# Optimization experiments

Hardware: AMD Instinct MI355X
Metric: run time of the kernel (lower is better)

Reference implementation:

```python
import jax, jax.numpy as jnp
import numpy as np

NU = 100_000   # users
NI = 100_000   # items
D  = 64        # embedding_size
NR = 1_000_000 # rate edges (user->item)
NL = 500_000   # link edges (user->user)
NEG_SLOPE = 0.2


def setup_inputs() -> dict:
    key = jax.random.key(0)
    ks = iter(jax.random.split(key, 40))
    s1 = 1.0 / np.sqrt(D)      # fan-in D
    s2 = 1.0 / np.sqrt(2 * D)  # fan-in 2D
    def nrm(shape, scale):
        return (jax.random.normal(next(ks), shape, jnp.float32) * scale).astype(jnp.float32)
    def idx(n, hi):
        return jax.random.randint(next(ks), (n,), 0, hi, jnp.int32)
    inp = {
        "user_emb": nrm((NU, D), 0.1),
        "item_emb": nrm((NI, D), 0.1),
        "rate_src": idx(NR, NU), "rate_dst": idx(NR, NI),
        "link_src": idx(NL, NU), "link_dst": idx(NL, NU),
        "neg_rate_src": idx(NR, NU), "neg_rate_dst": idx(NR, NI),
        "neg_link_src": idx(NL, NU), "neg_link_dst": idx(NL, NU),
        "lambda_max": jnp.full((), 2.0, jnp.float32),
        "gat_Wsrc": nrm((5, D, D), s1), "gat_bsrc": nrm((5, D), s1),
        "gat_Wdst": nrm((5, D, D), s1), "gat_bdst": nrm((5, D), s1),
        "gat_attn": nrm((5, D), s1),
        "W_out": nrm((2 * D, D), s2), "b_out": nrm((D,), s2),
        "cheb_W": nrm((3, D, D), s1), "cheb_b": nrm((D,), s1),
        "Wc": nrm((2 * D, D), s2), "bc": nrm((D,), s2),
        "Ws": nrm((2 * D, D), s2), "bs": nrm((D,), s2),
        "WpP": nrm((2 * D, D), s2), "bpP": nrm((D,), s2),
        "WpS": nrm((2 * D, D), s2), "bpS": nrm((D,), s2),
    }
    return inp


def _gatv2(Wsrc, bsrc, Wdst, bdst, attn, h_src, h_dst, src, dst, n_dst):
    """DGL GATv2Conv, num_heads=1, head dim squeezed. Returns [n_dst, D]."""
    fs = h_src @ Wsrc + bsrc            # [Ns, D]
    fd = h_dst @ Wdst + bdst            # [Nd, D]
    e = jax.nn.leaky_relu(fs[src] + fd[dst], NEG_SLOPE)  # [E, D]
    s = e @ attn                        # [E]
    m = jax.ops.segment_max(s, dst, num_segments=n_dst)
    ex = jnp.exp(s - m[dst])
    den = jax.ops.segment_sum(ex, dst, num_segments=n_dst)
    alpha = ex / den[dst]               # edge softmax per dst node
    return jax.ops.segment_sum(alpha[:, None] * fs[src], dst, num_segments=n_dst)


def _forward(user_emb, item_emb, rate_src, rate_dst, link_src, link_dst,
             neg_rate_src, neg_rate_dst, neg_link_src, neg_link_dst,
             lambda_max, gat_Wsrc, gat_bsrc, gat_Wdst, gat_bdst, gat_attn,
             W_out, b_out, cheb_W, cheb_b, Wc, bc, Ws, bs, WpP, bpP, WpS, bpS):
    def gat(i, h_src, h_dst, src, dst, n_dst):
        return _gatv2(gat_Wsrc[i], gat_bsrc[i], gat_Wdst[i], gat_bdst[i],
                      gat_attn[i], h_src, h_dst, src, dst, n_dst)

    # ---- SpatialAttentionLayer_GAT ----
    h1_item = gat(0, user_emb, item_emb, rate_src, rate_dst, NI)      # layer1[rate]
    h2_user = gat(1, item_emb, user_emb, rate_dst, rate_src, NU)      # layer1[rated-by]
    item_infl = gat(2, h1_item, user_emb, rate_dst, rate_src, NU)     # layer2[rated-by]
    social_item = gat(3, h2_user, user_emb, link_src, link_dst, NU)   # layer2[link]
    user_pref = jnp.concatenate([item_infl, social_item], axis=1) @ W_out + b_out

    # ---- SpectralAttentionLayer: ChebConv(k=3) on social graph + GATv2 ----
    indeg = jax.ops.segment_sum(jnp.ones((NL,), jnp.float32), link_dst, num_segments=NU)
    dinv = jnp.maximum(indeg, 1.0) ** -0.5
    def ahat(x):  # D^{-1/2} A D^{-1/2} x over link edges
        msg = (x * dinv[:, None])[link_src]
        return dinv[:, None] * jax.ops.segment_sum(msg, link_dst, num_segments=NU)
    re = 2.0 / lambda_max
    T0 = user_emb
    rst = T0 @ cheb_W[0]
    h = ahat(T0)
    T1 = -re * h + T0 * (re - 1.0)
    rst = rst + T1 @ cheb_W[1]
    h = ahat(T1)
    T2 = -2.0 * re * h + 2.0 * (re - 1.0) * T1 - T0
    rst = rst + T2 @ cheb_W[2] + cheb_b
    user_social = gat(4, rst, rst, link_src, link_dst, NU)

    # ---- MutualisicLayer ----
    h_uP = jnp.concatenate([user_pref, user_emb], axis=1) @ Wc + bc
    h_uS = jnp.concatenate([user_social, user_emb], axis=1) @ Ws + bs
    h_m = h_uP * h_uS
    h_mP = h_m * jax.nn.softmax(h_uP, axis=1)
    h_mS = h_m * jax.nn.softmax(h_uS, axis=1)
    h_miu_mP = jnp.concatenate([h_mP, h_uP], axis=1)
    h_miu_mS = jnp.concatenate([h_mS, h_uS], axis=1)

    # ---- PredictionLayer ----
    h_new_P = h_miu_mP @ WpP + bpP
    h_new_S = h_miu_mS @ WpS + bpS

    # ---- HeteroDotProductPredictor (u_dot_v per edge) ----
    pos_rate = jnp.sum(h_new_P[rate_src] * item_emb[rate_dst], axis=-1)
    neg_rate = jnp.sum(h_new_P[neg_rate_src] * item_emb[neg_rate_dst], axis=-1)
    pos_link = jnp.sum(h_new_S[link_src] * user_emb[link_dst], axis=-1)
    neg_link = jnp.sum(h_new_S[neg_link_src] * user_emb[neg_link_dst], axis=-1)
    return pos_rate, neg_rate, pos_link, neg_link


def reference(user_emb, item_emb, rate_src, rate_dst, link_src, link_dst,
              neg_rate_src, neg_rate_dst, neg_link_src, neg_link_dst,
              lambda_max, gat_Wsrc, gat_bsrc, gat_Wdst, gat_bdst, gat_attn,
              W_out, b_out, cheb_W, cheb_b, Wc, bc, Ws, bs, WpP, bpP, WpS, bpS):
    return _forward(user_emb, item_emb, rate_src, rate_dst, link_src, link_dst,
                    neg_rate_src, neg_rate_dst, neg_link_src, neg_link_dst,
                    lambda_max, gat_Wsrc, gat_bsrc, gat_Wdst, gat_bdst, gat_attn,
                    W_out, b_out, cheb_W, cheb_b, Wc, bc, Ws, bs, WpP, bpP, WpS, bpS)
```

## Files before the change

kernel.cpp:

```cpp
#include <hip/hip_runtime.h>


#define LRELU_SLOPE 0.2f
#define MFMA_BLOCKS 1024
#define EDGE_BLOCKS 2048

typedef unsigned short u16;
typedef unsigned int uint32;
typedef __attribute__((ext_vector_type(8))) short short8;
typedef __attribute__((ext_vector_type(4))) float f32x4;

__device__ __forceinline__ float b2f(u16 u) {
  return __uint_as_float(((uint32)u) << 16);
}
__device__ __forceinline__ u16 f2b(float f) {
  uint32 u = __float_as_uint(f);
  uint32 r = (u + 0x7fffu + ((u >> 16) & 1u)) >> 16;
  return (u16)r;
}
__device__ __forceinline__ float blo(uint32 p) { return __uint_as_float(p << 16); }
__device__ __forceinline__ float bhi(uint32 p) { return __uint_as_float(p & 0xffff0000u); }
__device__ __forceinline__ uint32 packb(float lo, float hi) {
  return (uint32)f2b(lo) | ((uint32)f2b(hi) << 16);
}

__global__ void cvt_k(const float4* __restrict__ X, ushort4* __restrict__ Y, int n4) {
  const int stride = gridDim.x * blockDim.x;
  for (int i = blockIdx.x * blockDim.x + threadIdx.x; i < n4; i += stride) {
    const float4 v = X[i];
    ushort4 o;
    o.x = f2b(v.x); o.y = f2b(v.y); o.z = f2b(v.z); o.w = f2b(v.w);
    Y[i] = o;
  }
}

__global__ void wfrag_k(const float* __restrict__ W, u16* __restrict__ fb, int nmat) {
  const int total = nmat * 4096;
  const int stride = gridDim.x * blockDim.x;
  for (int i = blockIdx.x * blockDim.x + threadIdx.x; i < total; i += stride) {
    const int mat = i >> 12, rem = i & 4095;
    const int l = rem >> 6, r = rem & 63;
    const int kc = r >> 5, cb = (r >> 3) & 3, j = r & 7;
    const int k = kc * 32 + ((l >> 4) & 3) * 8 + j;
    const int col = cb * 16 + (l & 15);
    fb[i] = f2b(W[(size_t)mat * 4096 + k * 64 + col]);
  }
}

template <int NIN>
__global__ void mfma_g_k(const u16* __restrict__ X0, const u16* __restrict__ X1,
                         const u16* __restrict__ X2,
                         const u16* __restrict__ F0, const u16* __restrict__ F1,
                         const u16* __restrict__ F2,
                         const float* __restrict__ b, u16* __restrict__ Y, int N) {
  const int lane = threadIdx.x & 63;
  const int gw = (blockIdx.x * blockDim.x + threadIdx.x) >> 6;
  const int nw = (gridDim.x * blockDim.x) >> 6;
  const int lo = lane & 15, hi = lane >> 4;
  short8 bf[NIN][2][4];
#pragma unroll
  for (int i = 0; i < NIN; ++i) {
    const u16* Fi = (i == 0) ? F0 : ((i == 1) ? F1 : F2);
#pragma unroll
    for (int kc = 0; kc < 2; ++kc)
#pragma unroll
      for (int cb = 0; cb < 4; ++cb)
        bf[i][kc][cb] = *(const short8*)(Fi + (size_t)lane * 64 + kc * 32 + cb * 8);
  }
  float bcol[4];
#pragma unroll
  for (int cb = 0; cb < 4; ++cb) bcol[cb] = b[cb * 16 + lo];
  const int ntile = (N + 15) >> 4;
  for (int t = gw; t < ntile; t += nw) {
    int arow = t * 16 + lo;
    if (arow >= N) arow = N - 1;
    f32x4 acc[4];
#pragma unroll
    for (int cb = 0; cb < 4; ++cb) {
      acc[cb][0] = bcol[cb]; acc[cb][1] = bcol[cb];
      acc[cb][2] = bcol[cb]; acc[cb][3] = bcol[cb];
    }
#pragma unroll
    for (int i = 0; i < NIN; ++i) {
      const u16* Xi = (i == 0) ? X0 : ((i == 1) ? X1 : X2);
      const short8 a0 = *(const short8*)(Xi + (size_t)arow * 64 + hi * 8);
      const short8 a1 = *(const short8*)(Xi + (size_t)arow * 64 + 32 + hi * 8);
#pragma unroll
      for (int cb = 0; cb < 4; ++cb)
        acc[cb] = __builtin_amdgcn_mfma_f32_16x16x32_bf16(a0, bf[i][0][cb], acc[cb], 0, 0, 0);
#pragma unroll
      for (int cb = 0; cb < 4; ++cb)
        acc[cb] = __builtin_amdgcn_mfma_f32_16x16x32_bf16(a1, bf[i][1][cb], acc[cb], 0, 0, 0);
    }
#pragma unroll
    for (int cb = 0; cb < 4; ++cb) {
#pragma unroll
      for (int j = 0; j < 4; ++j) {
        const int row = t * 16 + hi * 4 + j;
        if (row < N) Y[(size_t)row * 64 + cb * 16 + lo] = f2b(acc[cb][j]);
      }
    }
  }
}

__global__ void hist_k(const int* __restrict__ key, int* __restrict__ cnt, int E) {
  const int e = blockIdx.x * blockDim.x + threadIdx.x;
  if (e < E) atomicAdd(cnt + key[e], 1);
}

__global__ void scan1_k(const int* __restrict__ in, int* __restrict__ out,
                        int* __restrict__ bsum, int n) {
  __shared__ int tmp[256];
  const int t = threadIdx.x;
  const int base = blockIdx.x * 1024 + t * 4;
  int v0 = (base + 0 < n) ? in[base + 0] : 0;
  int v1 = (base + 1 < n) ? in[base + 1] : 0;
  int v2 = (base + 2 < n) ? in[base + 2] : 0;
  int v3 = (base + 3 < n) ? in[base + 3] : 0;
  const int s = v0 + v1 + v2 + v3;
  tmp[t] = s;
  __syncthreads();
  for (int off = 1; off < 256; off <<= 1) {
    const int x = (t >= off) ? tmp[t - off] : 0;
    __syncthreads();
    tmp[t] += x;
    __syncthreads();
  }
  const int excl = tmp[t] - s;
  if (t == 255) bsum[blockIdx.x] = tmp[255];
  if (base + 0 < n) out[base + 0] = excl;
  if (base + 1 < n) out[base + 1] = excl + v0;
  if (base + 2 < n) out[base + 2] = excl + v0 + v1;
  if (base + 3 < n) out[base + 3] = excl + v0 + v1 + v2;
}
__global__ void scan2_k(int* __restrict__ bsum, int nb) {
  if (threadIdx.x == 0) {
    int acc = 0;
    for (int i = 0; i < nb; ++i) { const int v = bsum[i]; bsum[i] = acc; acc += v; }
  }
}
__global__ void scan3_k(int* __restrict__ out, const int* __restrict__ bsum, int n) {
  const int i = blockIdx.x * blockDim.x + threadIdx.x;
  if (i < n) out[i] += bsum[i >> 10];
}

__global__ void scatter_k(const int* __restrict__ key, const int* __restrict__ other,
                          int* __restrict__ cursor, int* __restrict__ srt, int E) {
  const int e = blockIdx.x * blockDim.x + threadIdx.x;
  if (e < E) {
    const int p = atomicAdd(cursor + key[e], 1);
    srt[p] = other[e];
  }
}

__global__ void gat32_k(const u16* __restrict__ fs, const u16* __restrict__ fd,
                        const float* __restrict__ attn,
                        const int* __restrict__ rowptr, const int* __restrict__ nbr,
                        u16* __restrict__ out, int N) {
  const int lane = threadIdx.x & 63;
  const int l = lane & 31, half = lane >> 5;
  const int wid = (blockIdx.x * blockDim.x + threadIdx.x) >> 6;
  const int nw = (gridDim.x * blockDim.x) >> 6;
  const float awlo = attn[2 * l], awhi = attn[2 * l + 1];
  const uint32* fs32 = (const uint32*)fs;
  const uint32* fd32 = (const uint32*)fd;
  uint32* out32 = (uint32*)out;
  for (int n0 = wid * 2; n0 < N; n0 += nw * 2) {
    const int n = n0 + half;
    const bool act = n < N;
    const int beg = act ? rowptr[n] : 0;
    const int end = act ? rowptr[n + 1] : 0;
    float fdlo = 0.0f, fdhi = 0.0f;
    if (act) {
      const uint32 fp = fd32[(size_t)n * 32 + l];
      fdlo = blo(fp); fdhi = bhi(fp);
    }
    float aclo = 0.0f, achi = 0.0f, den = 0.0f;
    int e = beg;
    for (; e + 1 < end; e += 2) {
      const int s0 = nbr[e], s1 = nbr[e + 1];
      const uint32 f0 = fs32[(size_t)s0 * 32 + l];
      const uint32 f1 = fs32[(size_t)s1 * 32 + l];
      const float f0l = blo(f0), f0h = bhi(f0);
      const float f1l = blo(f1), f1h = bhi(f1);
      float v0l = f0l + fdlo; v0l = v0l > 0.0f ? v0l : LRELU_SLOPE * v0l;
      float v0h = f0h + fdhi; v0h = v0h > 0.0f ? v0h : LRELU_SLOPE * v0h;
      float v1l = f1l + fdlo; v1l = v1l > 0.0f ? v1l : LRELU_SLOPE * v1l;
      float v1h = f1h + fdhi; v1h = v1h > 0.0f ? v1h : LRELU_SLOPE * v1h;
      float p0 = fmaf(v0l, awlo, v0h * awhi);
      float p1 = fmaf(v1l, awlo, v1h * awhi);
#pragma unroll
      for (int o = 16; o; o >>= 1) {
        p0 += __shfl_xor(p0, o, 64);
        p1 += __shfl_xor(p1, o, 64);
      }
      const float e0 = __expf(p0), e1 = __expf(p1);
      den += e0 + e1;
      aclo = fmaf(e0, f0l, aclo); achi = fmaf(e0, f0h, achi);
      aclo = fmaf(e1, f1l, aclo); achi = fmaf(e1, f1h, achi);
    }
    if (e < end) {
      const int s0 = nbr[e];
      const uint32 f0 = fs32[(size_t)s0 * 32 + l];
      const float f0l = blo(f0), f0h = bhi(f0);
      float v0l = f0l + fdlo; v0l = v0l > 0.0f ? v0l : LRELU_SLOPE * v0l;
      float v0h = f0h + fdhi; v0h = v0h > 0.0f ? v0h : LRELU_SLOPE * v0h;
      float p0 = fmaf(v0l, awlo, v0h * awhi);
#pragma unroll
      for (int o = 16; o; o >>= 1) p0 += __shfl_xor(p0, o, 64);
      const float e0 = __expf(p0);
      den += e0;
      aclo = fmaf(e0, f0l, aclo); achi = fmaf(e0, f0h, achi);
    }
    const float inv = den > 0.0f ? 1.0f / den : 0.0f;
    if (act) out32[(size_t)n * 32 + l] = packb(aclo * inv, achi * inv);
  }
}

template <int MODE>
__global__ void cheb32_k(const u16* __restrict__ x, const u16* __restrict__ T0,
                         const u16* __restrict__ Tp, const float* __restrict__ dinv,
                         const float* __restrict__ lam,
                         const int* __restrict__ rowptr, const int* __restrict__ nbr,
                         u16* __restrict__ outT, int N) {
  const float re = 2.0f / lam[0];
  const int lane = threadIdx.x & 63;
  const int l = lane & 31, half = lane >> 5;
  const int wid = (blockIdx.x * blockDim.x + threadIdx.x) >> 6;
  const int nw = (gridDim.x * blockDim.x) >> 6;
  const uint32* x32 = (const uint32*)x;
  const uint32* T032 = (const uint32*)T0;
  const uint32* Tp32 = (const uint32*)Tp;
  uint32* o32 = (uint32*)outT;
  for (int n0 = wid * 2; n0 < N; n0 += nw * 2) {
    const int n = n0 + half;
    const bool act = n < N;
    const int beg = act ? rowptr[n] : 0;
    const int end = act ? rowptr[n + 1] : 0;
    float aclo = 0.0f, achi = 0.0f;
    int e = beg;
    for (; e + 1 < end; e += 2) {
      const int s0 = nbr[e], s1 = nbr[e + 1];
      const uint32 f0 = x32[(size_t)s0 * 32 + l];
      const uint32 f1 = x32[(size_t)s1 * 32 + l];
      const float d0 = dinv[s0], d1 = dinv[s1];
      aclo = fmaf(blo(f0), d0, aclo); achi = fmaf(bhi(f0), d0, achi);
      aclo = fmaf(blo(f1), d1, aclo); achi = fmaf(bhi(f1), d1, achi);
    }
    if (e < end) {
      const int s0 = nbr[e];
      const uint32 f0 = x32[(size_t)s0 * 32 + l];
      const float d0 = dinv[s0];
      aclo = fmaf(blo(f0), d0, aclo); achi = fmaf(bhi(f0), d0, achi);
    }
    if (!act) continue;
    const float dn = dinv[n];
    const float hl = aclo * dn, hh = achi * dn;
    float rl, rh;
    if (MODE == 1) {
      const uint32 t0 = T032[(size_t)n * 32 + l];
      rl = -re * hl + (re - 1.0f) * blo(t0);
      rh = -re * hh + (re - 1.0f) * bhi(t0);
    } else {
      const uint32 t0 = T032[(size_t)n * 32 + l];
      const uint32 tp = Tp32[(size_t)n * 32 + l];
      rl = -2.0f * re * hl + 2.0f * (re - 1.0f) * blo(tp) - blo(t0);
      rh = -2.0f * re * hh + 2.0f * (re - 1.0f) * bhi(tp) - bhi(t0);
    }
    o32[(size_t)n * 32 + l] = packb(rl, rh);
  }
}

__global__ void dinv_k(const int* __restrict__ rowptr, float* __restrict__ dinv, int N) {
  const int i = blockIdx.x * blockDim.x + threadIdx.x;
  if (i < N) {
    const float deg = (float)(rowptr[i + 1] - rowptr[i]);
    dinv[i] = rsqrtf(fmaxf(deg, 1.0f));
  }
}

__global__ void mut_k(const u16* __restrict__ hP, const u16* __restrict__ hS,
                      u16* __restrict__ mP, u16* __restrict__ mS, int N) {
  const int lane = threadIdx.x & 63;
  const int u = (blockIdx.x * blockDim.x + threadIdx.x) >> 6;
  if (u >= N) return;
  const float p = b2f(hP[(size_t)u * 64 + lane]);
  const float s = b2f(hS[(size_t)u * 64 + lane]);
  const float m = p * s;
  float mxp = p, mxs = s;
#pragma unroll
  for (int o = 32; o; o >>= 1) {
    mxp = fmaxf(mxp, __shfl_xor(mxp, o, 64));
    mxs = fmaxf(mxs, __shfl_xor(mxs, o, 64));
  }
  const float ep = __expf(p - mxp);
  const float es = __expf(s - mxs);
  float sp = ep, ss = es;
#pragma unroll
  for (int o = 32; o; o >>= 1) {
    sp += __shfl_xor(sp, o, 64);
    ss += __shfl_xor(ss, o, 64);
  }
  mP[(size_t)u * 64 + lane] = f2b(m * (ep / sp));
  mS[(size_t)u * 64 + lane] = f2b(m * (es / ss));
}

__global__ void dot32_k(const u16* __restrict__ A, const u16* __restrict__ Bm,
                        const int* __restrict__ src, const int* __restrict__ dst,
                        float* __restrict__ out, int E) {
  const int lane = threadIdx.x & 63;
  const int l = lane & 31, half = lane >> 5;
  const int wid = (blockIdx.x * blockDim.x + threadIdx.x) >> 6;
  const int nw = (gridDim.x * blockDim.x) >> 6;
  const uint32* A32 = (const uint32*)A;
  const uint32* B32 = (const uint32*)Bm;
  for (int e0 = wid * 4; e0 < E; e0 += nw * 4) {
    const int eA = e0 + half;
    const int eB = e0 + 2 + half;
    const int eAc = eA < E ? eA : E - 1;
    const int eBc = eB < E ? eB : E - 1;
    const int sA = src[eAc], dA = dst[eAc];
    const int sB = src[eBc], dB = dst[eBc];
    const uint32 a0 = A32[(size_t)sA * 32 + l];
    const uint32 b0 = B32[(size_t)dA * 32 + l];
    const uint32 a1 = A32[(size_t)sB * 32 + l];
    const uint32 b1 = B32[(size_t)dB * 32 + l];
    float p0 = fmaf(blo(a0), blo(b0), bhi(a0) * bhi(b0));
    float p1 = fmaf(blo(a1), blo(b1), bhi(a1) * bhi(b1));
#pragma unroll
    for (int o = 16; o; o >>= 1) {
      p0 += __shfl_xor(p0, o, 64);
      p1 += __shfl_xor(p1, o, 64);
    }
    if (l == 0) {
      if (eA < E) out[eA] = p0;
      if (eB < E) out[eB] = p1;
    }
  }
}


static void build_csr(const int* key, const int* other, int E, int N,
                      int* rowptr, int* srt, int* cursor, int* bsum,
                      hipStream_t stream) {
  const int n1 = N + 1;
  hipMemsetAsync(cursor, 0, (size_t)n1 * 4, stream);
  hist_k<<<(E + 255) / 256, 256, 0, stream>>>(key, cursor, E);
  const int nb = (n1 + 1023) / 1024;
  scan1_k<<<nb, 256, 0, stream>>>(cursor, rowptr, bsum, n1);
  scan2_k<<<1, 64, 0, stream>>>(bsum, nb);
  scan3_k<<<(n1 + 255) / 256, 256, 0, stream>>>(rowptr, bsum, n1);
  hipMemcpyAsync(cursor, rowptr, (size_t)N * 4, hipMemcpyDeviceToDevice, stream);
  scatter_k<<<(E + 255) / 256, 256, 0, stream>>>(key, other, cursor, srt, E);
}

extern "C" void kernel_launch(void* const* d_in, const int* in_sizes, int n_in,
                              void* d_out, int out_size, void* d_ws, size_t ws_size,
                              hipStream_t stream) {
  const float* user_emb = (const float*)d_in[0];
  const float* item_emb = (const float*)d_in[1];
  const int* rate_src = (const int*)d_in[2];
  const int* rate_dst = (const int*)d_in[3];
  const int* link_src = (const int*)d_in[4];
  const int* link_dst = (const int*)d_in[5];
  const int* neg_rate_src = (const int*)d_in[6];
  const int* neg_rate_dst = (const int*)d_in[7];
  const int* neg_link_src = (const int*)d_in[8];
  const int* neg_link_dst = (const int*)d_in[9];
  const float* lam = (const float*)d_in[10];
  const float* gat_Wsrc = (const float*)d_in[11];
  const float* gat_bsrc = (const float*)d_in[12];
  const float* gat_Wdst = (const float*)d_in[13];
  const float* gat_bdst = (const float*)d_in[14];
  const float* gat_attn = (const float*)d_in[15];
  const float* W_out = (const float*)d_in[16];
  const float* b_out = (const float*)d_in[17];
  const float* cheb_W = (const float*)d_in[18];
  const float* cheb_b = (const float*)d_in[19];
  const float* Wc = (const float*)d_in[20];
  const float* bc = (const float*)d_in[21];
  const float* Wsm = (const float*)d_in[22];
  const float* bs = (const float*)d_in[23];
  const float* WpP = (const float*)d_in[24];
  const float* bpP = (const float*)d_in[25];
  const float* WpS = (const float*)d_in[26];
  const float* bpS = (const float*)d_in[27];

  const int NU = in_sizes[0] / 64;
  const int NI = in_sizes[1] / 64;
  const int NR = in_sizes[2];
  const int NL = in_sizes[4];
  const int NMAX = NU > NI ? NU : NI;
  const size_t MAT = (size_t)NMAX * 64;
  const int FR = 4096;

  u16* ub = (u16*)d_ws;
  u16* ib = ub + (size_t)NU * 64;
  u16* B0 = ib + (size_t)NI * 64;
  u16* B1 = B0 + MAT;
  u16* B2 = B1 + MAT;
  u16* B3 = B2 + MAT;
  u16* B4 = B3 + MAT;
  u16* B5 = B4 + MAT;
  u16* B6 = B5 + MAT;
  u16* B7 = B6 + MAT;
  u16* fb = B7 + MAT;
  u16* fbWsrc = fb;
  u16* fbWdst = fb + 5 * FR;
  u16* fbWout = fb + 10 * FR;
  u16* fbCheb = fb + 12 * FR;
  u16* fbWc = fb + 15 * FR;
  u16* fbWsm = fb + 17 * FR;
  u16* fbWpP = fb + 19 * FR;
  u16* fbWpS = fb + 21 * FR;
  int* ip = (int*)(fb + 23 * FR);
  int* rp_rd = ip;
  int* rp_rs = rp_rd + (NI + 1);
  int* rp_ld = rp_rs + (NU + 1);
  int* srt_rd = rp_ld + (NU + 1);
  int* srt_rs = srt_rd + NR;
  int* srt_ld = srt_rs + NR;
  int* cursor = srt_ld + NL;
  int* bsum = cursor + (NMAX + 1);
  float* dinv = (float*)(bsum + 256);

  const int B64 = 64;

  cvt_k<<<1024, 256, 0, stream>>>((const float4*)user_emb, (ushort4*)ub, NU * 16);
  cvt_k<<<1024, 256, 0, stream>>>((const float4*)item_emb, (ushort4*)ib, NI * 16);
  wfrag_k<<<20, 256, 0, stream>>>(gat_Wsrc, fbWsrc, 5);
  wfrag_k<<<20, 256, 0, stream>>>(gat_Wdst, fbWdst, 5);
  wfrag_k<<<8, 256, 0, stream>>>(W_out, fbWout, 2);
  wfrag_k<<<12, 256, 0, stream>>>(cheb_W, fbCheb, 3);
  wfrag_k<<<8, 256, 0, stream>>>(Wc, fbWc, 2);
  wfrag_k<<<8, 256, 0, stream>>>(Wsm, fbWsm, 2);
  wfrag_k<<<8, 256, 0, stream>>>(WpP, fbWpP, 2);
  wfrag_k<<<8, 256, 0, stream>>>(WpS, fbWpS, 2);

  build_csr(rate_dst, rate_src, NR, NI, rp_rd, srt_rd, cursor, bsum, stream);
  build_csr(rate_src, rate_dst, NR, NU, rp_rs, srt_rs, cursor, bsum, stream);
  build_csr(link_dst, link_src, NL, NU, rp_ld, srt_ld, cursor, bsum, stream);

  mfma_g_k<1><<<MFMA_BLOCKS, 256, 0, stream>>>(ub, nullptr, nullptr,
      fbWsrc + 0 * FR, nullptr, nullptr, gat_bsrc + 0 * B64, B0, NU);
  mfma_g_k<1><<<MFMA_BLOCKS, 256, 0, stream>>>(ub, nullptr, nullptr,
      fbWdst + 1 * FR, nullptr, nullptr, gat_bdst + 1 * B64, B1, NU);
  mfma_g_k<1><<<MFMA_BLOCKS, 256, 0, stream>>>(ub, nullptr, nullptr,
      fbWdst + 2 * FR, nullptr, nullptr, gat_bdst + 2 * B64, B2, NU);
  mfma_g_k<1><<<MFMA_BLOCKS, 256, 0, stream>>>(ub, nullptr, nullptr,
      fbWdst + 3 * FR, nullptr, nullptr, gat_bdst + 3 * B64, B3, NU);
  mfma_g_k<1><<<MFMA_BLOCKS, 256, 0, stream>>>(ib, nullptr, nullptr,
      fbWdst + 0 * FR, nullptr, nullptr, gat_bdst + 0 * B64, B4, NI);
  mfma_g_k<1><<<MFMA_BLOCKS, 256, 0, stream>>>(ib, nullptr, nullptr,
      fbWsrc + 1 * FR, nullptr, nullptr, gat_bsrc + 1 * B64, B5, NI);

  gat32_k<<<EDGE_BLOCKS, 256, 0, stream>>>(B0, B4, gat_attn + 0 * B64, rp_rd, srt_rd, B6, NI);
  gat32_k<<<EDGE_BLOCKS, 256, 0, stream>>>(B5, B1, gat_attn + 1 * B64, rp_rs, srt_rs, B7, NU);

  mfma_g_k<1><<<MFMA_BLOCKS, 256, 0, stream>>>(B6, nullptr, nullptr,
      fbWsrc + 2 * FR, nullptr, nullptr, gat_bsrc + 2 * B64, B0, NI);
  gat32_k<<<EDGE_BLOCKS, 256, 0, stream>>>(B0, B2, gat_attn + 2 * B64, rp_rs, srt_rs, B4, NU);

  mfma_g_k<1><<<MFMA_BLOCKS, 256, 0, stream>>>(B7, nullptr, nullptr,
      fbWsrc + 3 * FR, nullptr, nullptr, gat_bsrc + 3 * B64, B5, NU);
  gat32_k<<<EDGE_BLOCKS, 256, 0, stream>>>(B5, B3, gat_attn + 3 * B64, rp_ld, srt_ld, B2, NU);

  mfma_g_k<2><<<MFMA_BLOCKS, 256, 0, stream>>>(B4, B2, nullptr,
      fbWout + 0 * FR, fbWout + 1 * FR, nullptr, b_out, B0, NU);

  dinv_k<<<(NU + 255) / 256, 256, 0, stream>>>(rp_ld, dinv, NU);
  cheb32_k<1><<<EDGE_BLOCKS, 256, 0, stream>>>(ub, ub, nullptr, dinv, lam,
                                               rp_ld, srt_ld, B5, NU);
  cheb32_k<2><<<EDGE_BLOCKS, 256, 0, stream>>>(B5, ub, B5, dinv, lam,
                                               rp_ld, srt_ld, B3, NU);
  mfma_g_k<3><<<MFMA_BLOCKS, 256, 0, stream>>>(ub, B5, B3,
      fbCheb + 0 * FR, fbCheb + 1 * FR, fbCheb + 2 * FR, cheb_b, B6, NU);

  mfma_g_k<1><<<MFMA_BLOCKS, 256, 0, stream>>>(B6, nullptr, nullptr,
      fbWsrc + 4 * FR, nullptr, nullptr, gat_bsrc + 4 * B64, B4, NU);
  mfma_g_k<1><<<MFMA_BLOCKS, 256, 0, stream>>>(B6, nullptr, nullptr,
      fbWdst + 4 * FR, nullptr, nullptr, gat_bdst + 4 * B64, B2, NU);
  gat32_k<<<EDGE_BLOCKS, 256, 0, stream>>>(B4, B2, gat_attn + 4 * B64, rp_ld, srt_ld, B5, NU);

  mfma_g_k<2><<<MFMA_BLOCKS, 256, 0, stream>>>(B0, ub, nullptr,
      fbWc + 0 * FR, fbWc + 1 * FR, nullptr, bc, B4, NU);
  mfma_g_k<2><<<MFMA_BLOCKS, 256, 0, stream>>>(B5, ub, nullptr,
      fbWsm + 0 * FR, fbWsm + 1 * FR, nullptr, bs, B2, NU);
  mut_k<<<(NU + 3) / 4, 256, 0, stream>>>(B4, B2, B3, B7, NU);
  mfma_g_k<2><<<MFMA_BLOCKS, 256, 0, stream>>>(B3, B4, nullptr,
      fbWpP + 0 * FR, fbWpP + 1 * FR, nullptr, bpP, B0, NU);
  mfma_g_k<2><<<MFMA_BLOCKS, 256, 0, stream>>>(B7, B2, nullptr,
      fbWpS + 0 * FR, fbWpS + 1 * FR, nullptr, bpS, B5, NU);

  float* out = (float*)d_out;
  dot32_k<<<EDGE_BLOCKS, 256, 0, stream>>>(B0, ib, rate_src, rate_dst, out, NR);
  dot32_k<<<EDGE_BLOCKS, 256, 0, stream>>>(B0, ib, neg_rate_src, neg_rate_dst, out + NR, NR);
  dot32_k<<<EDGE_BLOCKS, 256, 0, stream>>>(B5, ub, link_src, link_dst, out + 2 * (size_t)NR, NL);
  dot32_k<<<EDGE_BLOCKS, 256, 0, stream>>>(B5, ub, neg_link_src, neg_link_dst, out + 2 * (size_t)NR + NL, NL);
}
```

Baseline: 988.3 us.

## Fuse paired projections, dual CSR builds, and dot-product launches

Adds a dual-output MFMA projection kernel so one read of the input rows produces two linear projections, replacing six single GEMM launches with three and two with one. Builds the rate_src and rate_dst CSRs together with a combined histogram and scatter pass, reading the edge arrays once. Merges the pos/neg edge dot-product launches into one kernel each for rate and link. The aim is less redundant input traffic and fewer launches, at the cost of more registers per wave for the fused GEMM and extra branching in the dot kernel.

```diff
diff --git a/kernel.cpp b/kernel.cpp
--- a/kernel.cpp
+++ b/kernel.cpp
@@ -103,9 +103,69 @@
   }
 }
 
+__global__ void mfma_g2_k(const u16* __restrict__ X,
+                          const u16* __restrict__ F0, const u16* __restrict__ F1,
+                          const float* __restrict__ b0, const float* __restrict__ b1,
+                          u16* __restrict__ Y0, u16* __restrict__ Y1, int N) {
+  const int lane = threadIdx.x & 63;
+  const int gw = (blockIdx.x * blockDim.x + threadIdx.x) >> 6;
+  const int nw = (gridDim.x * blockDim.x) >> 6;
+  const int lo = lane & 15, hi = lane >> 4;
+  short8 bfA[2][4], bfB[2][4];
+#pragma unroll
+  for (int kc = 0; kc < 2; ++kc)
+#pragma unroll
+    for (int cb = 0; cb < 4; ++cb) {
+      bfA[kc][cb] = *(const short8*)(F0 + (size_t)lane * 64 + kc * 32 + cb * 8);
+      bfB[kc][cb] = *(const short8*)(F1 + (size_t)lane * 64 + kc * 32 + cb * 8);
+    }
+  float bc0[4], bc1[4];
+#pragma unroll
+  for (int cb = 0; cb < 4; ++cb) { bc0[cb] = b0[cb * 16 + lo]; bc1[cb] = b1[cb * 16 + lo]; }
+  const int ntile = (N + 15) >> 4;
+  for (int t = gw; t < ntile; t += nw) {
+    int arow = t * 16 + lo;
+    if (arow >= N) arow = N - 1;
+    const short8 a0 = *(const short8*)(X + (size_t)arow * 64 + hi * 8);
+    const short8 a1 = *(const short8*)(X + (size_t)arow * 64 + 32 + hi * 8);
+    f32x4 accA[4], accB[4];
+#pragma unroll
+    for (int cb = 0; cb < 4; ++cb) {
+      accA[cb][0] = bc0[cb]; accA[cb][1] = bc0[cb]; accA[cb][2] = bc0[cb]; accA[cb][3] = bc0[cb];
+      accB[cb][0] = bc1[cb]; accB[cb][1] = bc1[cb]; accB[cb][2] = bc1[cb]; accB[cb][3] = bc1[cb];
+    }
+#pragma unroll
+    for (int cb = 0; cb < 4; ++cb) {
+      accA[cb] = __builtin_amdgcn_mfma_f32_16x16x32_bf16(a0, bfA[0][cb], accA[cb], 0, 0, 0);
+      accA[cb] = __builtin_amdgcn_mfma_f32_16x16x32_bf16(a1, bfA[1][cb], accA[cb], 0, 0, 0);
+      accB[cb] = __builtin_amdgcn_mfma_f32_16x16x32_bf16(a0, bfB[0][cb], accB[cb], 0, 0, 0);
+      accB[cb] = __builtin_amdgcn_mfma_f32_16x16x32_bf16(a1, bfB[1][cb], accB[cb], 0, 0, 0);
+    }
+#pragma unroll
+    for (int cb = 0; cb < 4; ++cb) {
+#pragma unroll
+      for (int j = 0; j < 4; ++j) {
+        const int row = t * 16 + hi * 4 + j;
+        if (row < N) {
+          Y0[(size_t)row * 64 + cb * 16 + lo] = f2b(accA[cb][j]);
+          Y1[(size_t)row * 64 + cb * 16 + lo] = f2b(accB[cb][j]);
+        }
+      }
+    }
+  }
+}
+
 __global__ void hist_k(const int* __restrict__ key, int* __restrict__ cnt, int E) {
   const int e = blockIdx.x * blockDim.x + threadIdx.x;
   if (e < E) atomicAdd(cnt + key[e], 1);
+}
+__global__ void hist2_k(const int* __restrict__ src, const int* __restrict__ dst,
+                        int* __restrict__ cntS, int* __restrict__ cntD, int E) {
+  const int e = blockIdx.x * blockDim.x + threadIdx.x;
+  if (e < E) {
+    atomicAdd(cntS + src[e], 1);
+    atomicAdd(cntD + dst[e], 1);
+  }
 }
 
 __global__ void scan1_k(const int* __restrict__ in, int* __restrict__ out,
@@ -150,6 +210,18 @@
   if (e < E) {
     const int p = atomicAdd(cursor + key[e], 1);
     srt[p] = other[e];
+  }
+}
+__global__ void scatter2_k(const int* __restrict__ src, const int* __restrict__ dst,
+                           int* __restrict__ curS, int* __restrict__ curD,
+                           int* __restrict__ srtS, int* __restrict__ srtD, int E) {
+  const int e = blockIdx.x * blockDim.x + threadIdx.x;
+  if (e < E) {
+    const int s = src[e], d = dst[e];
+    const int p = atomicAdd(curD + d, 1);
+    srtD[p] = s;
+    const int q = atomicAdd(curS + s, 1);
+    srtS[q] = d;
   }
 }
 
@@ -305,22 +377,28 @@
   mS[(size_t)u * 64 + lane] = f2b(m * (es / ss));
 }
 
-__global__ void dot32_k(const u16* __restrict__ A, const u16* __restrict__ Bm,
-                        const int* __restrict__ src, const int* __restrict__ dst,
-                        float* __restrict__ out, int E) {
+__global__ void dot2_k(const u16* __restrict__ A, const u16* __restrict__ Bm,
+                       const int* __restrict__ src1, const int* __restrict__ dst1,
+                       float* __restrict__ out1, int E1,
+                       const int* __restrict__ src2, const int* __restrict__ dst2,
+                       float* __restrict__ out2, int E2) {
   const int lane = threadIdx.x & 63;
   const int l = lane & 31, half = lane >> 5;
   const int wid = (blockIdx.x * blockDim.x + threadIdx.x) >> 6;
   const int nw = (gridDim.x * blockDim.x) >> 6;
   const uint32* A32 = (const uint32*)A;
   const uint32* B32 = (const uint32*)Bm;
-  for (int e0 = wid * 4; e0 < E; e0 += nw * 4) {
-    const int eA = e0 + half;
-    const int eB = e0 + 2 + half;
-    const int eAc = eA < E ? eA : E - 1;
-    const int eBc = eB < E ? eB : E - 1;
-    const int sA = src[eAc], dA = dst[eAc];
-    const int sB = src[eBc], dB = dst[eBc];
+  const int total = E1 + E2;
+  for (int g0 = wid * 4; g0 < total; g0 += nw * 4) {
+    const int gA = g0 + half;
+    const int gB = g0 + 2 + half;
+    const int gAc = gA < total ? gA : total - 1;
+    const int gBc = gB < total ? gB : total - 1;
+    const bool a1st = gAc < E1, b1st = gBc < E1;
+    const int sA = a1st ? src1[gAc] : src2[gAc - E1];
+    const int dA = a1st ? dst1[gAc] : dst2[gAc - E1];
+    const int sB = b1st ? src1[gBc] : src2[gBc - E1];
+    const int dB = b1st ? dst1[gBc] : dst2[gBc - E1];
     const uint32 a0 = A32[(size_t)sA * 32 + l];
     const uint32 b0 = B32[(size_t)dA * 32 + l];
     const uint32 a1 = A32[(size_t)sB * 32 + l];
@@ -333,26 +411,16 @@
       p1 += __shfl_xor(p1, o, 64);
     }
     if (l == 0) {
-      if (eA < E) out[eA] = p0;
-      if (eB < E) out[eB] = p1;
-    }
-  }
-}
-
-
-static void build_csr(const int* key, const int* other, int E, int N,
-                      int* rowptr, int* srt, int* cursor, int* bsum,
-                      hipStream_t stream) {
-  const int n1 = N + 1;
-  hipMemsetAsync(cursor, 0, (size_t)n1 * 4, stream);
-  hist_k<<<(E + 255) / 256, 256, 0, stream>>>(key, cursor, E);
-  const int nb = (n1 + 1023) / 1024;
-  scan1_k<<<nb, 256, 0, stream>>>(cursor, rowptr, bsum, n1);
-  scan2_k<<<1, 64, 0, stream>>>(bsum, nb);
-  scan3_k<<<(n1 + 255) / 256, 256, 0, stream>>>(rowptr, bsum, n1);
-  hipMemcpyAsync(cursor, rowptr, (size_t)N * 4, hipMemcpyDeviceToDevice, stream);
-  scatter_k<<<(E + 255) / 256, 256, 0, stream>>>(key, other, cursor, srt, E);
-}
+      if (gA < total) {
+        if (a1st) out1[gA] = p0; else out2[gA - E1] = p0;
+      }
+      if (gB < total) {
+        if (b1st) out1[gB] = p1; else out2[gB - E1] = p1;
+      }
+    }
+  }
+}
+
 
 extern "C" void kernel_launch(void* const* d_in, const int* in_sizes, int n_in,
                               void* d_out, int out_size, void* d_ws, size_t ws_size,
@@ -420,8 +488,9 @@
   int* srt_rd = rp_ld + (NU + 1);
   int* srt_rs = srt_rd + NR;
   int* srt_ld = srt_rs + NR;
-  int* cursor = srt_ld + NL;
-  int* bsum = cursor + (NMAX + 1);
+  int* cursorA = srt_ld + NL;
+  int* cursorB = cursorA + (NMAX + 1);
+  int* bsum = cursorB + (NMAX + 1);
   float* dinv = (float*)(bsum + 256);
 
   const int B64 = 64;
@@ -437,22 +506,42 @@
   wfrag_k<<<8, 256, 0, stream>>>(WpP, fbWpP, 2);
   wfrag_k<<<8, 256, 0, stream>>>(WpS, fbWpS, 2);
 
-  build_csr(rate_dst, rate_src, NR, NI, rp_rd, srt_rd, cursor, bsum, stream);
-  build_csr(rate_src, rate_dst, NR, NU, rp_rs, srt_rs, cursor, bsum, stream);
-  build_csr(link_dst, link_src, NL, NU, rp_ld, srt_ld, cursor, bsum, stream);
-
-  mfma_g_k<1><<<MFMA_BLOCKS, 256, 0, stream>>>(ub, nullptr, nullptr,
-      fbWsrc + 0 * FR, nullptr, nullptr, gat_bsrc + 0 * B64, B0, NU);
-  mfma_g_k<1><<<MFMA_BLOCKS, 256, 0, stream>>>(ub, nullptr, nullptr,
-      fbWdst + 1 * FR, nullptr, nullptr, gat_bdst + 1 * B64, B1, NU);
-  mfma_g_k<1><<<MFMA_BLOCKS, 256, 0, stream>>>(ub, nullptr, nullptr,
-      fbWdst + 2 * FR, nullptr, nullptr, gat_bdst + 2 * B64, B2, NU);
-  mfma_g_k<1><<<MFMA_BLOCKS, 256, 0, stream>>>(ub, nullptr, nullptr,
-      fbWdst + 3 * FR, nullptr, nullptr, gat_bdst + 3 * B64, B3, NU);
-  mfma_g_k<1><<<MFMA_BLOCKS, 256, 0, stream>>>(ib, nullptr, nullptr,
-      fbWdst + 0 * FR, nullptr, nullptr, gat_bdst + 0 * B64, B4, NI);
-  mfma_g_k<1><<<MFMA_BLOCKS, 256, 0, stream>>>(ib, nullptr, nullptr,
-      fbWsrc + 1 * FR, nullptr, nullptr, gat_bsrc + 1 * B64, B5, NI);
+  hipMemsetAsync(cursorA, 0, (size_t)(NU + 1) * 4, stream);
+  hipMemsetAsync(cursorB, 0, (size_t)(NI + 1) * 4, stream);
+  hist2_k<<<(NR + 255) / 256, 256, 0, stream>>>(rate_src, rate_dst, cursorA, cursorB, NR);
+  {
+    const int n1 = NU + 1, nb = (n1 + 1023) / 1024;
+    scan1_k<<<nb, 256, 0, stream>>>(cursorA, rp_rs, bsum, n1);
+    scan2_k<<<1, 64, 0, stream>>>(bsum, nb);
+    scan3_k<<<(n1 + 255) / 256, 256, 0, stream>>>(rp_rs, bsum, n1);
+  }
+  {
+    const int n1 = NI + 1, nb = (n1 + 1023) / 1024;
+    scan1_k<<<nb, 256, 0, stream>>>(cursorB, rp_rd, bsum, n1);
+    scan2_k<<<1, 64, 0, stream>>>(bsum, nb);
+    scan3_k<<<(n1 + 255) / 256, 256, 0, stream>>>(rp_rd, bsum, n1);
+  }
+  hipMemcpyAsync(cursorA, rp_rs, (size_t)NU * 4, hipMemcpyDeviceToDevice, stream);
+  hipMemcpyAsync(cursorB, rp_rd, (size_t)NI * 4, hipMemcpyDeviceToDevice, stream);
+  scatter2_k<<<(NR + 255) / 256, 256, 0, stream>>>(rate_src, rate_dst, cursorA, cursorB,
+                                                   srt_rs, srt_rd, NR);
+  hipMemsetAsync(cursorA, 0, (size_t)(NU + 1) * 4, stream);
+  hist_k<<<(NL + 255) / 256, 256, 0, stream>>>(link_dst, cursorA, NL);
+  {
+    const int n1 = NU + 1, nb = (n1 + 1023) / 1024;
+    scan1_k<<<nb, 256, 0, stream>>>(cursorA, rp_ld, bsum, n1);
+    scan2_k<<<1, 64, 0, stream>>>(bsum, nb);
+    scan3_k<<<(n1 + 255) / 256, 256, 0, stream>>>(rp_ld, bsum, n1);
+  }
+  hipMemcpyAsync(cursorA, rp_ld, (size_t)NU * 4, hipMemcpyDeviceToDevice, stream);
+  scatter_k<<<(NL + 255) / 256, 256, 0, stream>>>(link_dst, link_src, cursorA, srt_ld, NL);
+
+  mfma_g2_k<<<MFMA_BLOCKS, 256, 0, stream>>>(ub, fbWsrc + 0 * FR, fbWdst + 1 * FR,
+      gat_bsrc + 0 * B64, gat_bdst + 1 * B64, B0, B1, NU);
+  mfma_g2_k<<<MFMA_BLOCKS, 256, 0, stream>>>(ub, fbWdst + 2 * FR, fbWdst + 3 * FR,
+      gat_bdst + 2 * B64, gat_bdst + 3 * B64, B2, B3, NU);
+  mfma_g2_k<<<MFMA_BLOCKS, 256, 0, stream>>>(ib, fbWdst + 0 * FR, fbWsrc + 1 * FR,
+      gat_bdst + 0 * B64, gat_bsrc + 1 * B64, B4, B5, NI);
 
   gat32_k<<<EDGE_BLOCKS, 256, 0, stream>>>(B0, B4, gat_attn + 0 * B64, rp_rd, srt_rd, B6, NI);
   gat32_k<<<EDGE_BLOCKS, 256, 0, stream>>>(B5, B1, gat_attn + 1 * B64, rp_rs, srt_rs, B7, NU);
@@ -476,10 +565,8 @@
   mfma_g_k<3><<<MFMA_BLOCKS, 256, 0, stream>>>(ub, B5, B3,
       fbCheb + 0 * FR, fbCheb + 1 * FR, fbCheb + 2 * FR, cheb_b, B6, NU);
 
-  mfma_g_k<1><<<MFMA_BLOCKS, 256, 0, stream>>>(B6, nullptr, nullptr,
-      fbWsrc + 4 * FR, nullptr, nullptr, gat_bsrc + 4 * B64, B4, NU);
-  mfma_g_k<1><<<MFMA_BLOCKS, 256, 0, stream>>>(B6, nullptr, nullptr,
-      fbWdst + 4 * FR, nullptr, nullptr, gat_bdst + 4 * B64, B2, NU);
+  mfma_g2_k<<<MFMA_BLOCKS, 256, 0, stream>>>(B6, fbWsrc + 4 * FR, fbWdst + 4 * FR,
+      gat_bsrc + 4 * B64, gat_bdst + 4 * B64, B4, B2, NU);
   gat32_k<<<EDGE_BLOCKS, 256, 0, stream>>>(B4, B2, gat_attn + 4 * B64, rp_ld, srt_ld, B5, NU);
 
   mfma_g_k<2><<<MFMA_BLOCKS, 256, 0, stream>>>(B0, ub, nullptr,
@@ -493,8 +580,8 @@
       fbWpS + 0 * FR, fbWpS + 1 * FR, nullptr, bpS, B5, NU);
 
   float* out = (float*)d_out;
-  dot32_k<<<EDGE_BLOCKS, 256, 0, stream>>>(B0, ib, rate_src, rate_dst, out, NR);
-  dot32_k<<<EDGE_BLOCKS, 256, 0, stream>>>(B0, ib, neg_rate_src, neg_rate_dst, out + NR, NR);
-  dot32_k<<<EDGE_BLOCKS, 256, 0, stream>>>(B5, ub, link_src, link_dst, out + 2 * (size_t)NR, NL);
-  dot32_k<<<EDGE_BLOCKS, 256, 0, stream>>>(B5, ub, neg_link_src, neg_link_dst, out + 2 * (size_t)NR + NL, NL);
-}
+  dot2_k<<<EDGE_BLOCKS, 256, 0, stream>>>(B0, ib, rate_src, rate_dst, out, NR,
+                                          neg_rate_src, neg_rate_dst, out + NR, NR);
+  dot2_k<<<EDGE_BLOCKS, 256, 0, stream>>>(B5, ub, link_src, link_dst, out + 2 * (size_t)NR, NL,
+                                          neg_link_src, neg_link_dst, out + 2 * (size_t)NR + NL, NL);
+}
```

After: 1.053 ms. +6.6%, slower.
